# Kernel optimization log

Hardware: AMD Instinct MI355X
Metric: run time of the kernel (lower is better)

The kernel has to match this reference:

```python
import jax, jax.numpy as jnp
import numpy as np

B, S, D, H, F = 2, 2048, 1024, 16, 4096
HD = D // H
EPS = 1e-5
NEG = -1e9


def _layernorm(x, g, b):
    mu = jnp.mean(x, axis=-1, keepdims=True)
    var = jnp.mean((x - mu) ** 2, axis=-1, keepdims=True)
    return (x - mu) * jax.lax.rsqrt(var + EPS) * g + b


def _attention(x, wq, wk, wv, wo, bo):
    b, s, d = x.shape
    q = (x @ wq).reshape(b, s, H, HD).transpose(0, 2, 1, 3)  # [b,h,s,hd]
    k = (x @ wk).reshape(b, s, H, HD).transpose(0, 2, 1, 3)
    v = (x @ wv).reshape(b, s, H, HD).transpose(0, 2, 1, 3)
    scores = jnp.einsum('bhqd,bhkd->bhqk', q, k) / (HD ** 0.5)
    # Faithful to source bug: masked_fill(mask == 0, -1e9) where mask = triu(diag=1)
    # -> positions with k <= q (lower triangle incl. diagonal) are filled with -1e9.
    lower = jnp.tril(jnp.ones((s, s), dtype=bool))
    scores = jnp.where(lower, NEG, scores)
    w = jax.nn.softmax(scores, axis=-1)
    o = jnp.einsum('bhqk,bhkd->bhqd', w, v)
    o = o.transpose(0, 2, 1, 3).reshape(b, s, d)
    return o @ wo + bo


def _ffn(x, w1, b1, w2, b2):
    return jax.nn.gelu(x @ w1 + b1, approximate=False) @ w2 + b2


def setup_inputs() -> dict:
    key = jax.random.key(0)
    ks = jax.random.split(key, 10)
    s = 0.02
    return {
        'x': jax.random.normal(ks[0], (B, S, D), jnp.float32),
        'wq': jax.random.normal(ks[1], (D, D), jnp.float32) * s,
        'wk': jax.random.normal(ks[2], (D, D), jnp.float32) * s,
        'wv': jax.random.normal(ks[3], (D, D), jnp.float32) * s,
        'wo': jax.random.normal(ks[4], (D, D), jnp.float32) * s,
        'bo': jnp.zeros((D,), jnp.float32),
        'ln1_g': jnp.ones((D,), jnp.float32),
        'ln1_b': jnp.zeros((D,), jnp.float32),
        'ln2_g': jnp.ones((D,), jnp.float32),
        'ln2_b': jnp.zeros((D,), jnp.float32),
        'w1': jax.random.normal(ks[5], (D, F), jnp.float32) * s,
        'b1': jnp.zeros((F,), jnp.float32),
        'w2': jax.random.normal(ks[6], (F, D), jnp.float32) * s,
        'b2': jnp.zeros((D,), jnp.float32),
    }


def reference(x, wq, wk, wv, wo, bo, ln1_g, ln1_b, ln2_g, ln2_b, w1, b1, w2, b2):
    shortcut = x
    h = _layernorm(x, ln1_g, ln1_b)
    h = _attention(h, wq, wk, wv, wo, bo)  # dropout = identity (eval)
    h = h + shortcut
    shortcut = h
    h2 = _layernorm(h, ln2_g, ln2_b)
    h2 = _attention(h2, wq, wk, wv, wo, bo)  # same attn module reused, per source
    h2 = _ffn(h2, w1, b1, w2, b2)
    return h2 + shortcut
```

## Files before the change

kernel.cpp:

```cpp
#include <hip/hip_runtime.h>
#include <hip/hip_bf16.h>
#include <math.h>

#define Bz 2
#define Sz 2048
#define Dz 1024
#define Hz 16
#define HDz 64
#define Fz 4096
#define ROWS (Bz*Sz)
#define EPSf 1e-5f
#define NEGf -1e9f
#define SC2f 0.1803368801111204f

typedef __attribute__((ext_vector_type(8))) short short8;
typedef __attribute__((ext_vector_type(4))) float floatx4;

__device__ __forceinline__ unsigned short f2bf(float f){
  __hip_bfloat16 h = __float2bfloat16(f);
  return *(unsigned short*)&h;
}
__device__ __forceinline__ float bf2f(unsigned short u){
  union { unsigned x; float f; } a; a.x = ((unsigned)u) << 16; return a.f;
}

__device__ __forceinline__ float fast_gelu(float x){
  float t  = fabsf(x) * 0.70710678118654752f;
  float kk = __builtin_amdgcn_rcpf(1.0f + 0.3275911f * t);
  float poly = ((((1.061405429f*kk - 1.453152027f)*kk + 1.421413741f)*kk
                 - 0.284496736f)*kk + 0.254829592f)*kk;
  float er = 1.0f - poly * __expf(-t*t);
  er = copysignf(er, x);
  return 0.5f * x * (1.0f + er);
}

__device__ __forceinline__ void gload16(const void* g, void* l){
  __builtin_amdgcn_global_load_lds(
      (const __attribute__((address_space(1))) unsigned int*)g,
      (__attribute__((address_space(3))) unsigned int*)l, 16, 0, 0);
}

__device__ __forceinline__ void bar(){
  asm volatile("" ::: "memory");
  __builtin_amdgcn_s_barrier();
  asm volatile("" ::: "memory");
}
#define WAITV6 asm volatile("s_waitcnt vmcnt(6)" ::: "memory")
#define WAITV0 asm volatile("s_waitcnt vmcnt(0)" ::: "memory")
#define WL0    asm volatile("s_waitcnt lgkmcnt(0)" ::: "memory")

__device__ __forceinline__ void xcd_remap(int& bmblk, int& bnblk){
  int gx = gridDim.x, gy = gridDim.y;
  int id = blockIdx.y * gx + blockIdx.x;
  int xcd = id & 7, local = id >> 3;
  bnblk = local % gx;
  bmblk = xcd * (gy >> 3) + local / gx;
}

__device__ __forceinline__ void tc_body(const float* __restrict__ W,
                                        unsigned short* __restrict__ Wt,
                                        int K, int N, int n0, int k0)
{
  __shared__ unsigned short Ts[32][33];
  int r = threadIdx.x >> 3, c0 = (threadIdx.x & 7) * 4;
  float4 w4 = *(const float4*)(W + (size_t)(k0+r)*N + n0 + c0);
  Ts[r][c0+0] = f2bf(w4.x); Ts[r][c0+1] = f2bf(w4.y);
  Ts[r][c0+2] = f2bf(w4.z); Ts[r][c0+3] = f2bf(w4.w);
  __syncthreads();
  unsigned v0 = Ts[c0+0][r], v1 = Ts[c0+1][r], v2 = Ts[c0+2][r], v3 = Ts[c0+3][r];
  uint2 p; p.x = v0 | (v1<<16); p.y = v2 | (v3<<16);
  *(uint2*)(Wt + (size_t)(n0+r)*K + k0 + c0) = p;
}

__global__ __launch_bounds__(256)
void transpose_qkvo(const float* __restrict__ w0, unsigned short* __restrict__ t0,
                    const float* __restrict__ w1, unsigned short* __restrict__ t1,
                    const float* __restrict__ w2, unsigned short* __restrict__ t2,
                    const float* __restrict__ w3, unsigned short* __restrict__ t3)
{
  int z = blockIdx.z;
  const float* W = z==0 ? w0 : z==1 ? w1 : z==2 ? w2 : w3;
  unsigned short* T = z==0 ? t0 : z==1 ? t1 : z==2 ? t2 : t3;
  tc_body(W, T, Dz, Dz, blockIdx.x*32, blockIdx.y*32);
}

__global__ __launch_bounds__(256)
void transpose_ffn(const float* __restrict__ w1, unsigned short* __restrict__ w1T,
                   const float* __restrict__ w2, unsigned short* __restrict__ w2T)
{
  int z = blockIdx.z;
  const float* W = z ? w2 : w1;
  unsigned short* T = z ? w2T : w1T;
  int K = z ? Fz : Dz, N = z ? Dz : Fz;
  int n0 = (z ? blockIdx.y : blockIdx.x) * 32;
  int k0 = (z ? blockIdx.x : blockIdx.y) * 32;
  tc_body(W, T, K, N, n0, k0);
}

__global__ __launch_bounds__(256)
void transpose_bf(const unsigned short* __restrict__ V, unsigned short* __restrict__ VT,
                  float* __restrict__ vsum)
{
  __shared__ unsigned short Ts[32][33];
  int st = blockIdx.x*32;
  int R0 = blockIdx.y*32;
  int b = R0 >> 10, hd0 = R0 & 1023;
  int r = threadIdx.x >> 3, c0 = (threadIdx.x & 7) * 4;
  uint2 w = *(const uint2*)(V + (size_t)(b*Sz + st + r)*Dz + hd0 + c0);
  Ts[r][c0+0] = (unsigned short)(w.x & 0xffff);
  Ts[r][c0+1] = (unsigned short)(w.x >> 16);
  Ts[r][c0+2] = (unsigned short)(w.y & 0xffff);
  Ts[r][c0+3] = (unsigned short)(w.y >> 16);
  __syncthreads();
  unsigned v0 = Ts[c0+0][r], v1 = Ts[c0+1][r], v2 = Ts[c0+2][r], v3 = Ts[c0+3][r];
  uint2 p; p.x = v0 | (v1<<16); p.y = v2 | (v3<<16);
  *(uint2*)(VT + (size_t)(R0+r)*Sz + st + c0) = p;
  float s = bf2f((unsigned short)v0) + bf2f((unsigned short)v1)
          + bf2f((unsigned short)v2) + bf2f((unsigned short)v3);
  s += __shfl_down(s, 1, 8);
  s += __shfl_down(s, 2, 8);
  s += __shfl_down(s, 4, 8);
  if ((threadIdx.x & 7) == 0) atomicAdd(vsum + R0 + r, s);
}

__global__ __launch_bounds__(256)
void ln_kernel(const float* __restrict__ in, const float* __restrict__ gam,
               const float* __restrict__ bet, unsigned short* __restrict__ out)
{
  int row = blockIdx.x, t = threadIdx.x;
  size_t base = (size_t)row * Dz;
  int c0 = t * 4;
  float4 x4 = *(const float4*)(in + base + c0);
  float v[4] = {x4.x, x4.y, x4.z, x4.w};
  float s = v[0]+v[1]+v[2]+v[3];
  #pragma unroll
  for (int off=32; off>0; off>>=1) s += __shfl_down(s, off, 64);
  __shared__ float ws[4];
  int lane = t & 63, wid = t >> 6;
  if (lane == 0) ws[wid] = s;
  __syncthreads();
  float mu = (ws[0]+ws[1]+ws[2]+ws[3]) * (1.0f/Dz);
  __syncthreads();
  float d0=v[0]-mu, d1=v[1]-mu, d2=v[2]-mu, d3=v[3]-mu;
  float s2 = d0*d0+d1*d1+d2*d2+d3*d3;
  #pragma unroll
  for (int off=32; off>0; off>>=1) s2 += __shfl_down(s2, off, 64);
  if (lane == 0) ws[wid] = s2;
  __syncthreads();
  float var = (ws[0]+ws[1]+ws[2]+ws[3]) * (1.0f/Dz);
  float rstd = rsqrtf(var + EPSf);
  float4 g4 = *(const float4*)(gam + c0);
  float4 b4 = *(const float4*)(bet + c0);
  unsigned r0 = f2bf((v[0]-mu)*rstd*g4.x + b4.x);
  unsigned r1 = f2bf((v[1]-mu)*rstd*g4.y + b4.y);
  unsigned r2 = f2bf((v[2]-mu)*rstd*g4.z + b4.z);
  unsigned r3 = f2bf((v[3]-mu)*rstd*g4.w + b4.w);
  uint2 p; p.x = r0 | (r1<<16); p.y = r2 | (r3<<16);
  *(uint2*)(out + base + c0) = p;
}

#define STG_A(buf, half, k0) { \
  _Pragma("unroll") for (int c_=0;c_<2;c_++){ \
    int sg_ = c_*8 + wave; \
    int row0_ = ((sg_>>3)<<7) + ((sg_&7)<<3) + ((half)<<6); \
    gload16(pA[half][c_] + (k0), &As[buf][row0_*64]); } }

#define STG_B(buf, jh, k0) { \
  _Pragma("unroll") for (int c_=0;c_<2;c_++){ \
    int sg_ = c_*8 + wave; int rho0_ = sg_<<3; \
    gload16(pB[jh][c_] + (k0), &Bs[buf][jh][rho0_*64]); } }

#define READ_A4(dst, buf, ihalf) { \
  _Pragma("unroll") for (int ii_=0; ii_<4; ++ii_){ \
    int row_ = wm*128 + ((ihalf)*4+ii_)*16 + l15; \
    _Pragma("unroll") for (int ks_=0; ks_<2; ++ks_){ \
      int slot_ = (ks_*4+quad) ^ (l15&7); \
      dst[ii_][ks_] = *(const short8*)&As[buf][row_*64 + slot_*8]; } } }

#define READ_B2(dst, buf, jh) { \
  _Pragma("unroll") for (int jl_=0; jl_<2; ++jl_){ \
    int rho_ = wn*32 + jl_*16 + l15; \
    _Pragma("unroll") for (int ks_=0; ks_<2; ++ks_){ \
      int slot_ = (ks_*4+quad) ^ (l15&7); \
      dst[jl_][ks_] = *(const short8*)&Bs[buf][jh][rho_*64 + slot_*8]; } } }

#define MFMA_PH(IH, JH, AF, BF) { \
  __builtin_amdgcn_s_setprio(1); \
  _Pragma("unroll") for (int ii_=0; ii_<4; ++ii_){ \
    _Pragma("unroll") for (int jl_=0; jl_<2; ++jl_){ \
      floatx4 c_ = acc[(IH)*4+ii_][(JH)*2+jl_]; \
      c_ = __builtin_amdgcn_mfma_f32_16x16x32_bf16(AF[ii_][0], BF[jl_][0], c_, 0,0,0); \
      c_ = __builtin_amdgcn_mfma_f32_16x16x32_bf16(AF[ii_][1], BF[jl_][1], c_, 0,0,0); \
      acc[(IH)*4+ii_][(JH)*2+jl_] = c_; } } \
  __builtin_amdgcn_s_setprio(0); }

__global__ __launch_bounds__(512, 2)
void gemm256(const unsigned short* __restrict__ A,
             const unsigned short* __restrict__ Bt,
             const float* __restrict__ bias, const float* __restrict__ res,
             float* __restrict__ outf, unsigned short* __restrict__ outb,
             int M, int N, int K, int lda, int ldb, int act, int qkvmode)
{
  __shared__ unsigned short As[2][256*64];
  __shared__ unsigned short Bs[2][2][128*64];

  int t = threadIdx.x;
  int wave = t >> 6, lane = t & 63;
  int l15 = lane & 15, quad = lane >> 4;
  int wm = wave >> 2, wn = wave & 3;

  int nN = gridDim.x, nM = gridDim.y;
  int id = blockIdx.y * nN + blockIdx.x;
  int xcd = id & 7, local = id >> 3;
  int bnblk = local % nN;
  int bmblk = xcd * (nM >> 3) + local / nN;
  int bm = bmblk * 256, bn = bnblk * 256;

  if (gridDim.z > 1){
    A    += (size_t)blockIdx.z * K;
    Bt   += (size_t)blockIdx.z * K;
    outf += (size_t)blockIdx.z * ((size_t)M * N);
  }

  int lrow = lane >> 3;
  int lcol = ((lane & 7) ^ (lane >> 3)) * 8;

  const unsigned short* pA[2][2];
  const unsigned short* pB[2][2];
  #pragma unroll
  for (int half=0; half<2; half++)
    #pragma unroll
    for (int c=0;c<2;c++){
      int sg = c*8 + wave;
      int row0 = ((sg>>3)<<7) + ((sg&7)<<3) + (half<<6);
      pA[half][c] = A + (size_t)(bm + row0 + lrow)*lda + lcol;
    }
  #pragma unroll
  for (int jh=0; jh<2; jh++)
    #pragma unroll
    for (int c=0;c<2;c++){
      int sg = c*8 + wave;
      int rho0 = sg<<3;
      int gn = ((rho0>>5)<<6) + (jh<<5) + (rho0&31);
      pB[jh][c] = Bt + (size_t)(bn + gn + lrow)*ldb + lcol;
    }

  floatx4 acc[8][4];
  #pragma unroll
  for (int i=0;i<8;i++)
    #pragma unroll
    for (int j=0;j<4;j++) acc[i][j] = (floatx4){0.f,0.f,0.f,0.f};

  STG_A(0, 0, 0);  STG_A(0, 1, 0);
  STG_B(0, 0, 0);  STG_B(0, 1, 0);
  STG_A(1, 0, 64); STG_A(1, 1, 64);
  STG_B(1, 0, 64);
  WAITV6;
  bar();

  int NKT = K >> 6;
  int nIter = NKT >> 1;
  for (int it = 0; it < nIter; ++it){
    bool more = (it + 1 < nIter);
    int k0B  = (2*it+1) << 6;
    int k0A2 = (2*it+2) << 6;
    int k0B2 = (2*it+3) << 6;
    short8 aLo[4][2], aHi[4][2], bcur[2][2];

    READ_A4(aLo, 0, 0);
    READ_B2(bcur, 0, 0);
    STG_B(1, 1, k0B);
    WL0; bar();
    MFMA_PH(0, 0, aLo, bcur);

    READ_A4(aHi, 0, 1);
    if (more) STG_A(0, 0, k0A2);
    WL0; bar();
    MFMA_PH(1, 0, aHi, bcur);

    READ_B2(bcur, 0, 1);
    if (more) STG_A(0, 1, k0A2);
    WL0; bar();
    MFMA_PH(1, 1, aHi, bcur);

    if (more) { STG_B(0, 0, k0A2); WAITV6; }
    else      { WAITV0; }
    bar();
    MFMA_PH(0, 1, aLo, bcur);

    READ_A4(aLo, 1, 0);
    READ_B2(bcur, 1, 0);
    if (more) STG_B(0, 1, k0A2);
    WL0; bar();
    MFMA_PH(0, 0, aLo, bcur);

    READ_A4(aHi, 1, 1);
    if (more) STG_A(1, 0, k0B2);
    WL0; bar();
    MFMA_PH(1, 0, aHi, bcur);

    READ_B2(bcur, 1, 1);
    if (more) STG_A(1, 1, k0B2);
    WL0; bar();
    MFMA_PH(1, 1, aHi, bcur);

    if (more) { STG_B(1, 0, k0B2); WAITV6; }
    bar();
    MFMA_PH(0, 1, aLo, bcur);
  }

  float bj[4];
  #pragma unroll
  for (int j=0;j<4;j++) bj[j] = bias ? bias[bn + wn*64 + j*16 + l15] : 0.f;

  size_t selbase = 0; int ncol = N; int bnl = bn;
  if (qkvmode){ selbase = (size_t)(bn >> 10) * ((size_t)M * 1024); ncol = 1024; bnl = bn & 1023; }

  #pragma unroll
  for (int i=0;i<8;i++){
    int row0 = bm + wm*128 + i*16 + quad*4;
    #pragma unroll
    for (int r=0;r<4;r++){
      size_t rowoff = selbase + (size_t)(row0 + r) * ncol;
      #pragma unroll
      for (int j=0;j<4;j++){
        float v = acc[i][j][r] + bj[j];
        if (act) v = fast_gelu(v);
        size_t off = rowoff + bnl + wn*64 + j*16 + l15;
        if (res) v += res[off];
        if (outf) outf[off] = v;
        else      outb[off] = f2bf(v);
      }
    }
  }
}

__global__ __launch_bounds__(256)
void gemm_n64(const unsigned short* __restrict__ A,
              const unsigned short* __restrict__ Bt,
              const float* __restrict__ bias, const float* __restrict__ res,
              float* __restrict__ outf, unsigned short* __restrict__ outb,
              int M, int N, int K)
{
  __shared__ unsigned short As[2][128*64];
  __shared__ unsigned short Bs[2][64*64];
  int t = threadIdx.x;
  int bmblk, bnblk; xcd_remap(bmblk, bnblk);
  int bm = bmblk * 128, bn = bnblk * 64;
  int wave = t >> 6, lane = t & 63;
  int l15 = lane & 15, quad = lane >> 4;
  int arow = lane >> 3;
  int acbg = ((lane & 7) ^ arow) * 8;
  const unsigned short* gA = A  + (size_t)(bm + wave*32 + arow)*K + acbg;
  const unsigned short* gB = Bt + (size_t)(bn + wave*16 + arow)*K + acbg;

  floatx4 acc[2][4];
  #pragma unroll
  for (int i=0;i<2;i++)
    #pragma unroll
    for (int j=0;j<4;j++) acc[i][j] = (floatx4){0.f,0.f,0.f,0.f};

  int swr = (l15 & 7);

  {
    unsigned short* lA = &As[0][wave*32*64];
    unsigned short* lB = &Bs[0][wave*16*64];
    gload16(gA,                 lA);
    gload16(gA + (size_t)8*K,   lA + 8*64);
    gload16(gA + (size_t)16*K,  lA + 16*64);
    gload16(gA + (size_t)24*K,  lA + 24*64);
    gload16(gB,                 lB);
    gload16(gB + (size_t)8*K,   lB + 8*64);
  }

  int nIter = K >> 6;
  for (int it = 0; it < nIter; ++it) {
    __syncthreads();
    int cur = it & 1;
    if (it + 1 < nIter) {
      int k1 = (it+1) << 6;
      unsigned short* lA = &As[cur^1][wave*32*64];
      unsigned short* lB = &Bs[cur^1][wave*16*64];
      gload16(gA + k1,                 lA);
      gload16(gA + k1 + (size_t)8*K,   lA + 8*64);
      gload16(gA + k1 + (size_t)16*K,  lA + 16*64);
      gload16(gA + k1 + (size_t)24*K,  lA + 24*64);
      gload16(gB + k1,                 lB);
      gload16(gB + k1 + (size_t)8*K,   lB + 8*64);
    }
    const unsigned short* Ac = As[cur];
    const unsigned short* Bc = Bs[cur];
    #pragma unroll
    for (int ks=0; ks<2; ++ks){
      short8 af[2], bf[4];
      #pragma unroll
      for (int i=0;i<2;i++)
        af[i] = *(const short8*)&Ac[(wave*32 + i*16 + l15)*64 + ((ks*4 + quad) ^ swr)*8];
      #pragma unroll
      for (int j=0;j<4;j++)
        bf[j] = *(const short8*)&Bc[(j*16 + l15)*64 + ((ks*4 + quad) ^ swr)*8];
      #pragma unroll
      for (int i=0;i<2;i++)
        #pragma unroll
        for (int j=0;j<4;j++)
          acc[i][j] = __builtin_amdgcn_mfma_f32_16x16x32_bf16(af[i], bf[j], acc[i][j], 0, 0, 0);
    }
  }

  float bj[4];
  #pragma unroll
  for (int j=0;j<4;j++) bj[j] = bias ? bias[bn + j*16 + l15] : 0.f;

  #pragma unroll
  for (int i=0;i<2;i++){
    int row0 = bm + wave*32 + i*16 + quad*4;
    #pragma unroll
    for (int r=0;r<4;r++){
      size_t rowoff = (size_t)(row0 + r) * N;
      #pragma unroll
      for (int j=0;j<4;j++){
        float v = acc[i][j][r] + bj[j];
        size_t off = rowoff + bn + j*16 + l15;
        if (res) v += res[off];
        if (outf) outf[off] = v;
        else      outb[off] = f2bf(v);
      }
    }
  }
}

__global__ __launch_bounds__(256)
void reduce4(const float* __restrict__ part, const float* __restrict__ bias,
             const float* __restrict__ res, float* __restrict__ out)
{
  const size_t NN = (size_t)ROWS * Dz;
  size_t i = ((size_t)blockIdx.x * 256 + threadIdx.x) * 4;
  float4 a = *(const float4*)(part + i);
  float4 b = *(const float4*)(part + NN + i);
  float4 c = *(const float4*)(part + 2*NN + i);
  float4 d = *(const float4*)(part + 3*NN + i);
  float4 r = *(const float4*)(res + i);
  int col = threadIdx.x * 4;
  float4 g = *(const float4*)(bias + col);
  float4 o;
  o.x = a.x+b.x+c.x+d.x + g.x + r.x;
  o.y = a.y+b.y+c.y+d.y + g.y + r.y;
  o.z = a.z+b.z+c.z+d.z + g.z + r.z;
  o.w = a.w+b.w+c.w+d.w + g.w + r.w;
  *(float4*)(out + i) = o;
}

#define ATT_STAGE_KV() { \
    *(uint4*)&Ks[sr*64 + ((kc2  ) ^ ksw)*8] = pk0; \
    *(uint4*)&Ks[sr*64 + ((kc2+1) ^ ksw)*8] = pk1; \
    *(uint4*)&Vts[vd*128 + (((vk8  )&8) | (((vk8  )^vsw)&7))*8] = pv0; \
    *(uint4*)&Vts[vd*128 + (((vk8+1)&8) | (((vk8+1)^vsw)&7))*8] = pv1; }

#define ATT_PREFETCH(tile) { \
    size_t off0_ = ((size_t)(b*Sz + (tile)*128 + sr))*Dz + h*HDz + sc; \
    pk0 = *(const uint4*)(Kg + off0_); pk1 = *(const uint4*)(Kg + off0_ + 8); \
    int vo_ = (tile)*128 + vc*16; \
    pv0 = *(const uint4*)(vrow + vo_); pv1 = *(const uint4*)(vrow + vo_ + 8); }

#define ATT_COMPUTE(MASKED) { \
  _Pragma("unroll") \
  for (int hh=0; hh<2; ++hh){ \
    floatx4 acc_s[4]; \
    _Pragma("unroll") for (int j=0;j<4;j++) acc_s[j] = (floatx4){0.f,0.f,0.f,0.f}; \
    __builtin_amdgcn_s_setprio(1); \
    _Pragma("unroll") \
    for (int ks=0;ks<2;ks++){ \
      short8 bk[4]; \
      _Pragma("unroll") \
      for (int j=0;j<4;j++) \
        bk[j] = *(const short8*)&Ks[(hh*64 + j*16 + l15)*64 + (((ks*4+quad) ^ (l15&7)))*8]; \
      _Pragma("unroll") \
      for (int j=0;j<4;j++) \
        acc_s[j] = __builtin_amdgcn_mfma_f32_16x16x32_bf16(aq[ks], bk[j], acc_s[j], 0, 0, 0); \
    } \
    __builtin_amdgcn_s_setprio(0); \
    _Pragma("unroll") \
    for (int j=0;j<4;j++){ \
      _Pragma("unroll") \
      for (int r=0;r<4;r++){ \
        float s2 = acc_s[j][r] * SC2f; \
        if (MASKED){ int kloc = hh*64 + j*16 + l15; if (kloc <= qloc + r) s2 = NEGf; } \
        float p = __builtin_amdgcn_exp2f(fminf(s2, 115.41f)); \
        lacc[r] += p; \
        Ps[wave*16 + quad*4 + r][j*16 + l15] = f2bf(p); \
      } \
    } \
    __builtin_amdgcn_s_setprio(1); \
    _Pragma("unroll") \
    for (int ks=0;ks<2;ks++){ \
      short8 ap, bv[4]; \
      ap = *(const short8*)&Ps[wave*16 + l15][ks*32 + quad*8]; \
      _Pragma("unroll") \
      for (int j=0;j<4;j++) \
        bv[j] = *(const short8*)&Vts[(j*16 + l15)*128 + (hh*8 + ((ks*4+quad) ^ (l15&7)))*8]; \
      _Pragma("unroll") \
      for (int j=0;j<4;j++) \
        acc_o[j] = __builtin_amdgcn_mfma_f32_16x16x32_bf16(ap, bv[j], acc_o[j], 0, 0, 0); \
    } \
    __builtin_amdgcn_s_setprio(0); \
  } }

__global__ __launch_bounds__(512, 4)
void attn_mfma(const unsigned short* __restrict__ Qg,
               const unsigned short* __restrict__ Kg,
               const unsigned short* __restrict__ VTg,
               const float* __restrict__ vmean,
               unsigned short* __restrict__ Og)
{
  __shared__ unsigned short Ks[128*64];
  __shared__ unsigned short Vts[64*128];
  __shared__ unsigned short Ps[128][72];

  int t = threadIdx.x;
  int wave = t >> 6, lane = t & 63;
  int l15 = lane & 15, quad = lane >> 4;
  int b = blockIdx.z, h = blockIdx.y;
  int qt = b ? (15 - (int)blockIdx.x) : (int)blockIdx.x;

  {
    int r = t >> 2, c = (t & 3) * 16;
    const unsigned short* qp = Qg + ((size_t)(b*Sz + qt*128 + r))*Dz + h*HDz + c;
    uint4 q0 = *(const uint4*)(qp);
    uint4 q1 = *(const uint4*)(qp + 8);
    *(uint4*)&Ps[r][c]     = q0;
    *(uint4*)&Ps[r][c + 8] = q1;
  }

  int sr = t >> 2, sc = (t & 3) * 16;
  int kc2 = (t & 3) * 2, ksw = sr & 7;
  int vd = t >> 3, vc = t & 7, vsw = vd & 7;
  int vk8 = vc * 2;
  const unsigned short* vrow = VTg + ((size_t)((b*Hz + h)*64 + vd))*Sz;

  uint4 pk0, pk1, pv0, pv1;
  ATT_PREFETCH(qt);

  __syncthreads();
  short8 aq[2];
  aq[0] = *(const short8*)&Ps[wave*16 + l15][quad*8];
  aq[1] = *(const short8*)&Ps[wave*16 + l15][32 + quad*8];

  floatx4 acc_o[4];
  #pragma unroll
  for (int j=0;j<4;j++) acc_o[j] = (floatx4){0.f,0.f,0.f,0.f};
  float lacc[4] = {0.f, 0.f, 0.f, 0.f};

  int qloc = wave*16 + quad*4;

  ATT_STAGE_KV();
  __syncthreads();
  if (qt + 1 < Sz/128) ATT_PREFETCH(qt+1);
  ATT_COMPUTE(1);

  for (int jt2 = qt+1; jt2 < Sz/128; ++jt2){
    __syncthreads();
    ATT_STAGE_KV();
    __syncthreads();
    if (jt2 + 1 < Sz/128) ATT_PREFETCH(jt2+1);
    ATT_COMPUTE(0);
  }

  #pragma unroll
  for (int r=0;r<4;r++){
    float l = lacc[r];
    l += __shfl_xor(l, 1, 64);
    l += __shfl_xor(l, 2, 64);
    l += __shfl_xor(l, 4, 64);
    l += __shfl_xor(l, 8, 64);
    int qrow = qt*128 + wave*16 + quad*4 + r;
    float inv = 1.0f / l;
    size_t rowoff = ((size_t)(b*Sz + qrow))*Dz + h*HDz;
    #pragma unroll
    for (int j=0;j<4;j++){
      float ov = acc_o[j][r] * inv;
      if (qrow == Sz-1) ov = vmean[(b*Hz + h)*HDz + j*16 + l15] * (1.0f/2048.0f);
      Og[rowoff + j*16 + l15] = f2bf(ov);
    }
  }
}

extern "C" void kernel_launch(void* const* d_in, const int* in_sizes, int n_in,
                              void* d_out, int out_size, void* d_ws, size_t ws_size,
                              hipStream_t stream)
{
  const float* x    = (const float*)d_in[0];
  const float* wq   = (const float*)d_in[1];
  const float* wk   = (const float*)d_in[2];
  const float* wv   = (const float*)d_in[3];
  const float* wo   = (const float*)d_in[4];
  const float* bo   = (const float*)d_in[5];
  const float* ln1g = (const float*)d_in[6];
  const float* ln1b = (const float*)d_in[7];
  const float* ln2g = (const float*)d_in[8];
  const float* ln2b = (const float*)d_in[9];
  const float* w1   = (const float*)d_in[10];
  const float* b1   = (const float*)d_in[11];
  const float* w2   = (const float*)d_in[12];
  const float* b2   = (const float*)d_in[13];
  float* out = (float*)d_out;

  const size_t MB = 1024*1024;
  char* w = (char*)d_ws;
  float*          trunk = (float*)(w);
  unsigned short* lnb   = (unsigned short*)(w + 16*MB);
  unsigned short* q     = (unsigned short*)(w + 24*MB);
  unsigned short* k     = (unsigned short*)(w + 32*MB);
  unsigned short* v     = (unsigned short*)(w + 40*MB);
  unsigned short* ctx   = (unsigned short*)(w + 48*MB);
  unsigned short* wqkvT = (unsigned short*)(w + 56*MB);
  unsigned short* wqT   = wqkvT;
  unsigned short* wkT   = (unsigned short*)(w + 58*MB);
  unsigned short* wvT   = (unsigned short*)(w + 60*MB);
  unsigned short* woT   = (unsigned short*)(w + 62*MB);
  unsigned short* w1T   = (unsigned short*)(w + 64*MB);
  unsigned short* w2T   = (unsigned short*)(w + 72*MB);
  unsigned short* mid   = (unsigned short*)(w + 24*MB);
  float*          part  = (float*)(w + 80*MB);
  bool splitk = ws_size >= (size_t)144*MB;

  unsigned short* vT    = (unsigned short*)d_out;
  float*          vmean = (float*)((char*)d_out + 8*MB);

  dim3 blk(256), blk512(512);
  transpose_qkvo<<<dim3(32,32,4), blk, 0, stream>>>(wq, wqT, wk, wkT, wv, wvT, wo, woT);
  transpose_ffn<<<dim3(128,32,2), blk, 0, stream>>>(w1, w1T, w2, w2T);

  dim3 gln(ROWS);
  dim3 gqkv(3*Dz/256, ROWS/256);
  dim3 gf1(Fz/256,  ROWS/256);
  dim3 gn64(Dz/64,  ROWS/128);
  dim3 gattn(Sz/128, Hz, Bz);
  dim3 gvt(Sz/32, Bz*Hz*HDz/32);

  ln_kernel<<<gln, blk, 0, stream>>>(x, ln1g, ln1b, lnb);
  gemm256<<<gqkv, blk512, 0, stream>>>(lnb, wqkvT, nullptr, nullptr, nullptr, q, ROWS, 3*Dz, Dz, Dz, Dz, 0, 1);
  hipMemsetAsync(vmean, 0, 2048*sizeof(float), stream);
  transpose_bf<<<gvt, blk, 0, stream>>>(v, vT, vmean);
  attn_mfma<<<gattn, blk512, 0, stream>>>(q, k, vT, vmean, ctx);
  gemm_n64<<<gn64, blk, 0, stream>>>(ctx, woT, bo, x, trunk, nullptr, ROWS, Dz, Dz);

  ln_kernel<<<gln, blk, 0, stream>>>(trunk, ln2g, ln2b, lnb);
  gemm256<<<gqkv, blk512, 0, stream>>>(lnb, wqkvT, nullptr, nullptr, nullptr, q, ROWS, 3*Dz, Dz, Dz, Dz, 0, 1);
  hipMemsetAsync(vmean, 0, 2048*sizeof(float), stream);
  transpose_bf<<<gvt, blk, 0, stream>>>(v, vT, vmean);
  attn_mfma<<<gattn, blk512, 0, stream>>>(q, k, vT, vmean, ctx);
  gemm_n64<<<gn64, blk, 0, stream>>>(ctx, woT, bo, nullptr, nullptr, lnb, ROWS, Dz, Dz);
  gemm256<<<gf1, blk512, 0, stream>>>(lnb, w1T, b1, nullptr, nullptr, mid, ROWS, Fz, Dz, Dz, Dz, 1, 0);
  if (splitk) {
    gemm256<<<dim3(4,16,4), blk512, 0, stream>>>(mid, w2T, nullptr, nullptr, part, nullptr, ROWS, Dz, Fz/4, Fz, Fz, 0, 0);
    reduce4<<<dim3(4096), blk, 0, stream>>>(part, b2, trunk, out);
  } else {
    gemm_n64<<<gn64, blk, 0, stream>>>(mid, w2T, b2, trunk, out, nullptr, ROWS, Dz, Fz);
  }
}
```

Before: 453.0 us.

## Restructure GEMM main loop into four phases with both B halves held in registers

The GEMM K-loop changes from eight barrier-separated phases to four. Each phase reads both B sub-tiles into registers and issues two MFMA groups per barrier, and the prefetch order of A and B global-to-LDS loads is reshuffled with a vmcnt(4) wait instead of vmcnt(6). The aim is to halve the barrier count per iteration and give more MFMA work between syncs. The cost is higher register pressure from the extra B fragments, and the new load/wait ordering could expose more memory latency or create a hazard if the counts are wrong.

```diff
diff --git a/kernel.cpp b/kernel.cpp
--- a/kernel.cpp
+++ b/kernel.cpp
@@ -45,7 +45,7 @@
   __builtin_amdgcn_s_barrier();
   asm volatile("" ::: "memory");
 }
-#define WAITV6 asm volatile("s_waitcnt vmcnt(6)" ::: "memory")
+#define WAITV4 asm volatile("s_waitcnt vmcnt(4)" ::: "memory")
 #define WAITV0 asm volatile("s_waitcnt vmcnt(0)" ::: "memory")
 #define WL0    asm volatile("s_waitcnt lgkmcnt(0)" ::: "memory")
 
@@ -253,9 +253,8 @@
 
   STG_A(0, 0, 0);  STG_A(0, 1, 0);
   STG_B(0, 0, 0);  STG_B(0, 1, 0);
-  STG_A(1, 0, 64); STG_A(1, 1, 64);
-  STG_B(1, 0, 64);
-  WAITV6;
+  STG_B(1, 0, 64); STG_B(1, 1, 64);
+  WAITV4;
   bar();
 
   int NKT = K >> 6;
@@ -265,48 +264,36 @@
     int k0B  = (2*it+1) << 6;
     int k0A2 = (2*it+2) << 6;
     int k0B2 = (2*it+3) << 6;
-    short8 aLo[4][2], aHi[4][2], bcur[2][2];
+    short8 aLo[4][2], aHi[4][2], b01[2][2], b23[2][2];
 
     READ_A4(aLo, 0, 0);
-    READ_B2(bcur, 0, 0);
-    STG_B(1, 1, k0B);
+    READ_B2(b01, 0, 0);
+    READ_B2(b23, 0, 1);
+    STG_A(1, 0, k0B); STG_A(1, 1, k0B);
     WL0; bar();
-    MFMA_PH(0, 0, aLo, bcur);
+    MFMA_PH(0, 0, aLo, b01);
+    MFMA_PH(0, 1, aLo, b23);
 
     READ_A4(aHi, 0, 1);
-    if (more) STG_A(0, 0, k0A2);
+    if (more) { STG_A(0, 0, k0A2); STG_B(0, 0, k0A2); WAITV4; }
+    else      { WAITV0; }
     WL0; bar();
-    MFMA_PH(1, 0, aHi, bcur);
-
-    READ_B2(bcur, 0, 1);
-    if (more) STG_A(0, 1, k0A2);
+    MFMA_PH(1, 0, aHi, b01);
+    MFMA_PH(1, 1, aHi, b23);
+
+    READ_A4(aLo, 1, 0);
+    READ_B2(b01, 1, 0);
+    READ_B2(b23, 1, 1);
+    if (more) { STG_A(0, 1, k0A2); STG_B(0, 1, k0A2); }
     WL0; bar();
-    MFMA_PH(1, 1, aHi, bcur);
-
-    if (more) { STG_B(0, 0, k0A2); WAITV6; }
-    else      { WAITV0; }
-    bar();
-    MFMA_PH(0, 1, aLo, bcur);
-
-    READ_A4(aLo, 1, 0);
-    READ_B2(bcur, 1, 0);
-    if (more) STG_B(0, 1, k0A2);
+    MFMA_PH(0, 0, aLo, b01);
+    MFMA_PH(0, 1, aLo, b23);
+
+    READ_A4(aHi, 1, 1);
+    if (more) { STG_B(1, 0, k0B2); STG_B(1, 1, k0B2); WAITV4; }
     WL0; bar();
-    MFMA_PH(0, 0, aLo, bcur);
-
-    READ_A4(aHi, 1, 1);
-    if (more) STG_A(1, 0, k0B2);
-    WL0; bar();
-    MFMA_PH(1, 0, aHi, bcur);
-
-    READ_B2(bcur, 1, 1);
-    if (more) STG_A(1, 1, k0B2);
-    WL0; bar();
-    MFMA_PH(1, 1, aHi, bcur);
-
-    if (more) { STG_B(1, 0, k0B2); WAITV6; }
-    bar();
-    MFMA_PH(0, 1, aLo, bcur);
+    MFMA_PH(1, 0, aHi, b01);
+    MFMA_PH(1, 1, aHi, b23);
   }
 
   float bj[4];
```

After: 439.9 us. 2.9% less time.
